# Kernel optimization log

Hardware: AMD Instinct MI355X
Metric: run time of the kernel (lower is better)

The kernel has to match this reference:

```python
import jax, jax.numpy as jnp
import numpy as np

N_NODES = 100000
N_EDGES = 1600000
F_IN, F_HID, F_OUT = 256, 128, 32


def setup_inputs() -> dict:
    key = jax.random.key(0)
    k1, k2, k3, k4 = jax.random.split(key, 4)
    x = jax.random.normal(k1, (N_NODES, F_IN), dtype=jnp.float32)
    edge_index = jax.random.randint(k2, (2, N_EDGES), 0, N_NODES, dtype=jnp.int64)
    W1 = jax.random.normal(k3, (F_IN, F_HID), dtype=jnp.float32) * (1.0 / np.sqrt(F_IN))
    b1 = jnp.zeros((F_HID,), dtype=jnp.float32)
    W2 = jax.random.normal(k4, (F_HID, F_OUT), dtype=jnp.float32) * (1.0 / np.sqrt(F_HID))
    b2 = jnp.zeros((F_OUT,), dtype=jnp.float32)
    return {"x": x, "edge_index": edge_index, "W1": W1, "b1": b1, "W2": W2, "b2": b2}


def _gcn_norm(edge_index, num_nodes):
    # Add self-loops, then symmetric normalization deg^-1/2[src] * deg^-1/2[dst].
    loops = jnp.arange(num_nodes, dtype=edge_index.dtype)
    src = jnp.concatenate([edge_index[0], loops])
    dst = jnp.concatenate([edge_index[1], loops])
    deg = jax.ops.segment_sum(jnp.ones_like(dst, dtype=jnp.float32), dst,
                              num_segments=num_nodes)
    dinv = jnp.where(deg > 0, jax.lax.rsqrt(deg), 0.0)
    norm = dinv[src] * dinv[dst]  # [E + N]
    return src, dst, norm


def _gcn_conv(h, src, dst, norm, num_nodes):
    # h already linearly transformed. Gather sources, scale, scatter-add to dst.
    msgs = h[src] * norm[:, None]
    return jax.ops.segment_sum(msgs, dst, num_segments=num_nodes)


def reference(x, edge_index, W1, b1, W2, b2):
    n = x.shape[0]
    src, dst, norm = _gcn_norm(edge_index, n)
    # Layer 1: linear -> normalized scatter-add -> bias -> relu
    h = _gcn_conv(x @ W1, src, dst, norm, n) + b1
    h = jax.nn.relu(h)
    # F.dropout with training=False (eval mode) is identity.
    # Layer 2
    out = _gcn_conv(h @ W2, src, dst, norm, n) + b2
    return jax.nn.log_softmax(out, axis=1)
```

## Files before the change

kernel.cpp:

```cpp
#include <hip/hip_runtime.h>

#define N_NODES 100000
#define N_EDGES 1600000
#define F_IN 256
#define F_HID 128
#define F_OUT 32
#define NBUCK 391
#define BIN_BLOCKS 512
#define EDGES_PER_BIN 3125
#define G1_BLOCKS 1563

typedef unsigned short ushort_t;
typedef unsigned int uint_t;

using short8  = __attribute__((ext_vector_type(8))) short;
using floatx4 = __attribute__((ext_vector_type(4))) float;

__device__ __forceinline__ ushort_t f2bf(float f) {
    uint_t u = __float_as_uint(f);
    u += 0x7fff + ((u >> 16) & 1);
    return (ushort_t)(u >> 16);
}
__device__ __forceinline__ float bf_lo(uint_t u) { return __uint_as_float(u << 16); }
__device__ __forceinline__ float bf_hi(uint_t u) { return __uint_as_float(u & 0xffff0000u); }
__device__ __forceinline__ uint_t bfpack_trunc(float a, float b) {
    return __builtin_amdgcn_perm(__float_as_uint(b), __float_as_uint(a), 0x07060302u);
}

__global__ __launch_bounds__(256) void histwt_kernel(const int* __restrict__ ei,
                                                     int* __restrict__ bucket_cnt,
                                                     const float* __restrict__ W1,
                                                     const float* __restrict__ W2,
                                                     ushort_t* __restrict__ W1T,
                                                     ushort_t* __restrict__ W2T) {
    __shared__ int h[NBUCK];
    if (blockIdx.x < BIN_BLOCKS) {
        for (int i = threadIdx.x; i < NBUCK; i += 256) h[i] = 0;
        __syncthreads();
        int gid = blockIdx.x * 256 + threadIdx.x;
        for (int e = gid; e < N_EDGES; e += BIN_BLOCKS * 256)
            atomicAdd(&h[ei[N_EDGES + e] >> 8], 1);
        __syncthreads();
        for (int i = threadIdx.x; i < NBUCK; i += 256) {
            int c = h[i];
            if (c) atomicAdd(&bucket_cnt[i], c);
        }
    } else {
        int t = (blockIdx.x - BIN_BLOCKS) * 256 + threadIdx.x;
#pragma unroll
        for (int j = 0; j < 4; j++) {
            int e = j * 8192 + t;
            int n = e >> 8, k = e & 255;
            W1T[e] = f2bf(W1[k * F_HID + n]);
        }
        if (t < 4096) {
            int n = t >> 7, k = t & 127;
            W2T[t] = f2bf(W2[k * F_OUT + n]);
        }
    }
}

__global__ __launch_bounds__(512) void scan_kernel(const int* __restrict__ bucket_cnt,
                                                   int* __restrict__ bucket_base,
                                                   int* __restrict__ bucket_cursor,
                                                   int* __restrict__ offs) {
    __shared__ int s[512];
    int t = threadIdx.x;
    int own = (t < NBUCK) ? bucket_cnt[t] : 0;
    s[t] = own;
    __syncthreads();
    for (int off = 1; off < 512; off <<= 1) {
        int v = (t >= off) ? s[t - off] : 0;
        __syncthreads();
        s[t] += v;
        __syncthreads();
    }
    if (t < NBUCK) {
        int ex = s[t] - own;
        bucket_base[t] = ex;
        bucket_cursor[t] = ex;
    }
    if (t == 0) {
        bucket_base[NBUCK] = N_EDGES;
        offs[N_NODES] = N_EDGES;
    }
}

__global__ __launch_bounds__(256) void bin_gemm1_kernel(const int* __restrict__ ei,
                                                        int* __restrict__ bucket_cursor,
                                                        int2* __restrict__ binned,
                                                        const float* __restrict__ x,
                                                        const ushort_t* __restrict__ W1T,
                                                        ushort_t* __restrict__ h0a,
                                                        ushort_t* __restrict__ h0b) {
    __shared__ __align__(16) char smem[(size_t)F_HID * 136 * 2];
    const int tid = threadIdx.x;
    if (blockIdx.x < BIN_BLOCKS) {
        int* h    = (int*)smem;
        int* base = ((int*)smem) + NBUCK;
        const int beg = blockIdx.x * EDGES_PER_BIN;
        const int end = beg + EDGES_PER_BIN;
        for (int i = tid; i < NBUCK; i += 256) h[i] = 0;
        __syncthreads();
        for (int e = beg + tid; e < end; e += 256) atomicAdd(&h[ei[N_EDGES + e] >> 8], 1);
        __syncthreads();
        for (int i = tid; i < NBUCK; i += 256) {
            int c = h[i];
            base[i] = c ? atomicAdd(&bucket_cursor[i], c) : 0;
            h[i] = 0;
        }
        __syncthreads();
        for (int e = beg + tid; e < end; e += 256) {
            int s = ei[e], d = ei[N_EDGES + e];
            int bk = d >> 8;
            int p = base[bk] + atomicAdd(&h[bk], 1);
            binned[p] = make_int2(s, d);
        }
    } else {
        ushort_t (*Bst)[136] = (ushort_t(*)[136])smem;
        const int rbase = (blockIdx.x - BIN_BLOCKS) * 64;
        const int w = tid >> 6;
        const int lane = tid & 63;
        const int q = lane >> 4;
        const int nloc = lane & 15;

        const int rowA = rbase + w * 16 + nloc;
        const bool okA = rowA < N_NODES;
        const float* ap = x + (size_t)rowA * F_IN + q * 8;

        floatx4 acc[8];
#pragma unroll
        for (int t = 0; t < 8; t++) acc[t] = (floatx4){0.f, 0.f, 0.f, 0.f};

#pragma unroll
        for (int half = 0; half < 2; half++) {
#pragma unroll
            for (int j = 0; j < 8; j++) {
                int f = j * 256 + tid;
                int n = f >> 4, kg = f & 15;
                uint4 v = ((const uint4*)(W1T + n * F_IN + half * 128))[kg];
                *(uint4*)(&Bst[n][kg * 8]) = v;
            }
            __syncthreads();

#pragma unroll
            for (int k0 = 0; k0 < 128; k0 += 32) {
                float4 f0 = make_float4(0.f, 0.f, 0.f, 0.f);
                float4 f1 = make_float4(0.f, 0.f, 0.f, 0.f);
                if (okA) {
                    f0 = *(const float4*)(ap + half * 128 + k0);
                    f1 = *(const float4*)(ap + half * 128 + k0 + 4);
                }
                uint4 au;
                au.x = bfpack_trunc(f0.x, f0.y);
                au.y = bfpack_trunc(f0.z, f0.w);
                au.z = bfpack_trunc(f1.x, f1.y);
                au.w = bfpack_trunc(f1.z, f1.w);
                short8 a = *(short8*)&au;
#pragma unroll
                for (int t = 0; t < 8; t++) {
                    short8 b = *(const short8*)(&Bst[t * 16 + nloc][k0 + q * 8]);
                    acc[t] = __builtin_amdgcn_mfma_f32_16x16x32_bf16(a, b, acc[t], 0, 0, 0);
                }
            }
            __syncthreads();
        }

#pragma unroll
        for (int reg = 0; reg < 4; reg++) {
            int rowD = rbase + w * 16 + q * 4 + reg;
            if (rowD < N_NODES) {
                ushort_t* opA = h0a + (size_t)rowD * 64 + nloc;
                ushort_t* opB = h0b + (size_t)rowD * 64 + nloc;
#pragma unroll
                for (int t = 0; t < 4; t++) opA[t * 16] = f2bf(acc[t][reg]);
#pragma unroll
                for (int t = 4; t < 8; t++) opB[(t - 4) * 16] = f2bf(acc[t][reg]);
            }
        }
    }
}

__global__ __launch_bounds__(256) void build_kernel(const int2* __restrict__ binned,
                                                    const int* __restrict__ bucket_base,
                                                    int* __restrict__ offs,
                                                    int* __restrict__ csr,
                                                    float* __restrict__ dinv,
                                                    int* __restrict__ degarr) {
    __shared__ int h[256];
    __shared__ int sc[256];
    __shared__ int cur[256];
    const int b = blockIdx.x, t = threadIdx.x;
    const int beg = bucket_base[b];
    const int end = bucket_base[b + 1];
    h[t] = 0;
    __syncthreads();
    for (int j = beg + t; j < end; j += 256) {
        int2 p = binned[j];
        atomicAdd(&h[p.y & 255], 1);
    }
    __syncthreads();
    int deg = h[t];
    sc[t] = deg;
    __syncthreads();
    for (int off = 1; off < 256; off <<= 1) {
        int v = (t >= off) ? sc[t - off] : 0;
        __syncthreads();
        sc[t] += v;
        __syncthreads();
    }
    int excl = sc[t] - deg;
    cur[t] = excl;
    int node = b * 256 + t;
    if (node < N_NODES) {
        offs[node] = beg + excl;
        dinv[node] = rsqrtf((float)deg + 1.0f);
        degarr[node] = deg;
    }
    __syncthreads();
    for (int j = beg + t; j < end; j += 256) {
        int2 p = binned[j];
        int pos = atomicAdd(&cur[p.y & 255], 1);
        csr[beg + pos] = p.x;
    }
}

__global__ __launch_bounds__(256) void pack_kernel(int* __restrict__ csr,
                                                   const int* __restrict__ degarr) {
    int i = blockIdx.x * 256 + threadIdx.x;
    if (i >= N_EDGES / 4) return;
    int4 c = ((int4*)csr)[i];
    c.x |= degarr[c.x] << 20;
    c.y |= degarr[c.y] << 20;
    c.z |= degarr[c.z] << 20;
    c.w |= degarr[c.w] << 20;
    ((int4*)csr)[i] = c;
}

__global__ __launch_bounds__(256) void gather64(const ushort_t* __restrict__ h0a,
                                                const ushort_t* __restrict__ h0b,
                                                const int* __restrict__ offs,
                                                const int* __restrict__ csr,
                                                const float* __restrict__ dinv,
                                                ushort_t* __restrict__ aggA,
                                                ushort_t* __restrict__ aggB) {
    const int half = blockIdx.x >= (N_NODES / 8);
    const int nb = blockIdx.x - half * (N_NODES / 8);
    const ushort_t* tab = half ? h0b : h0a;
    ushort_t* outt = half ? aggB : aggA;

    const int node = nb * 8 + (threadIdx.x >> 5);
    const int l = threadIdx.x & 31;
    const int sub = l >> 3;
    const int fl = l & 7;
    const float dn = dinv[node];
    const uint4* rowbase = (const uint4*)tab;

    uint4 sv = rowbase[(size_t)node * 8 + fl];
    float s = (sub == 0) ? dn * dn : 0.f;
    float a[8];
    a[0] = bf_lo(sv.x) * s; a[1] = bf_hi(sv.x) * s;
    a[2] = bf_lo(sv.y) * s; a[3] = bf_hi(sv.y) * s;
    a[4] = bf_lo(sv.z) * s; a[5] = bf_hi(sv.z) * s;
    a[6] = bf_lo(sv.w) * s; a[7] = bf_hi(sv.w) * s;

    const int beg = offs[node], end = offs[node + 1];
    for (int j = beg; j < end; j += 16) {
        uint_t w[4];
        float nn[4];
        uint4 r[4];
#pragma unroll
        for (int k = 0; k < 4; k++) w[k] = ((const uint_t*)csr)[j + 4 * k + sub];
#pragma unroll
        for (int k = 0; k < 4; k++) {
            bool v = (j + 4 * k + sub) < end;
            int src = v ? (int)(w[k] & 0xFFFFFu) : 0;
            nn[k] = v ? rsqrtf((float)(w[k] >> 20) + 1.0f) * dn : 0.f;
            r[k] = rowbase[(size_t)src * 8 + fl];
        }
#pragma unroll
        for (int k = 0; k < 4; k++) {
            float n = nn[k];
            a[0] += bf_lo(r[k].x) * n; a[1] += bf_hi(r[k].x) * n;
            a[2] += bf_lo(r[k].y) * n; a[3] += bf_hi(r[k].y) * n;
            a[4] += bf_lo(r[k].z) * n; a[5] += bf_hi(r[k].z) * n;
            a[6] += bf_lo(r[k].w) * n; a[7] += bf_hi(r[k].w) * n;
        }
    }
#pragma unroll
    for (int i = 0; i < 8; i++) {
        a[i] += __shfl_xor(a[i], 8);
        a[i] += __shfl_xor(a[i], 16);
    }
    if (sub == 0) {
        uint4 p;
        p.x = (uint_t)f2bf(a[0]) | ((uint_t)f2bf(a[1]) << 16);
        p.y = (uint_t)f2bf(a[2]) | ((uint_t)f2bf(a[3]) << 16);
        p.z = (uint_t)f2bf(a[4]) | ((uint_t)f2bf(a[5]) << 16);
        p.w = (uint_t)f2bf(a[6]) | ((uint_t)f2bf(a[7]) << 16);
        ((uint4*)outt)[(size_t)node * 8 + fl] = p;
    }
}

__global__ __launch_bounds__(256) void gemm2_kernel(const ushort_t* __restrict__ aggA,
                                                    const ushort_t* __restrict__ aggB,
                                                    const float* __restrict__ b1,
                                                    const ushort_t* __restrict__ W2T,
                                                    ushort_t* __restrict__ h2bf) {
    __shared__ ushort_t Bs[F_OUT][F_HID + 8];
    __shared__ float b1s[F_HID];
    const int tid = threadIdx.x;
    const int rbase = blockIdx.x * 64;
    const int w = tid >> 6;
    const int lane = tid & 63;
    const int q = lane >> 4;
    const int nloc = lane & 15;

    if (tid < F_HID) b1s[tid] = b1[tid];
#pragma unroll
    for (int jj = 0; jj < 2; jj++) {
        int f = jj * 256 + tid;
        int n = f >> 4, kg = f & 15;
        uint4 v = ((const uint4*)(W2T + n * F_HID))[kg];
        *(uint4*)(&Bs[n][kg * 8]) = v;
    }
    __syncthreads();

    const int rowA = rbase + w * 16 + nloc;
    const bool okA = rowA < N_NODES;

    floatx4 acc[2];
    acc[0] = (floatx4){0.f, 0.f, 0.f, 0.f};
    acc[1] = (floatx4){0.f, 0.f, 0.f, 0.f};

#pragma unroll
    for (int k0 = 0; k0 < F_HID; k0 += 32) {
        int kk = k0 + q * 8;
        const ushort_t* at = (k0 < 64) ? aggA : aggB;
        int kloc = (k0 < 64) ? kk : kk - 64;
        uint4 av = make_uint4(0, 0, 0, 0);
        if (okA) av = *(const uint4*)(at + (size_t)rowA * 64 + kloc);
        float4 bb0 = *(const float4*)(&b1s[kk]);
        float4 bb1 = *(const float4*)(&b1s[kk + 4]);
        uint4 au;
        au.x = bfpack_trunc(fmaxf(bf_lo(av.x) + bb0.x, 0.f), fmaxf(bf_hi(av.x) + bb0.y, 0.f));
        au.y = bfpack_trunc(fmaxf(bf_lo(av.y) + bb0.z, 0.f), fmaxf(bf_hi(av.y) + bb0.w, 0.f));
        au.z = bfpack_trunc(fmaxf(bf_lo(av.z) + bb1.x, 0.f), fmaxf(bf_hi(av.z) + bb1.y, 0.f));
        au.w = bfpack_trunc(fmaxf(bf_lo(av.w) + bb1.z, 0.f), fmaxf(bf_hi(av.w) + bb1.w, 0.f));
        short8 a = *(short8*)&au;
#pragma unroll
        for (int t = 0; t < 2; t++) {
            short8 b = *(const short8*)(&Bs[t * 16 + nloc][kk]);
            acc[t] = __builtin_amdgcn_mfma_f32_16x16x32_bf16(a, b, acc[t], 0, 0, 0);
        }
    }
#pragma unroll
    for (int reg = 0; reg < 4; reg++) {
        int rowD = rbase + w * 16 + q * 4 + reg;
        if (rowD < N_NODES) {
            ushort_t* op = h2bf + (size_t)rowD * F_OUT + nloc;
            op[0]  = f2bf(acc[0][reg]);
            op[16] = f2bf(acc[1][reg]);
        }
    }
}

__global__ __launch_bounds__(256) void gather32_lsm(const ushort_t* __restrict__ h2bf,
                                                    const int* __restrict__ offs,
                                                    const int* __restrict__ csr,
                                                    const float* __restrict__ dinv,
                                                    const float* __restrict__ b2,
                                                    float* __restrict__ out) {
    const int node = blockIdx.x * 8 + (threadIdx.x >> 5);
    const int l = threadIdx.x & 31;
    const int sub = l >> 2;
    const int fl = l & 3;
    const float dn = dinv[node];
    const uint4* rowbase = (const uint4*)h2bf;

    uint4 sv = rowbase[(size_t)node * 4 + fl];
    float s = (sub == 0) ? dn * dn : 0.f;
    float a[8];
    a[0] = bf_lo(sv.x) * s; a[1] = bf_hi(sv.x) * s;
    a[2] = bf_lo(sv.y) * s; a[3] = bf_hi(sv.y) * s;
    a[4] = bf_lo(sv.z) * s; a[5] = bf_hi(sv.z) * s;
    a[6] = bf_lo(sv.w) * s; a[7] = bf_hi(sv.w) * s;

    const int beg = offs[node], end = offs[node + 1];
    for (int j = beg; j < end; j += 16) {
        uint_t w[2];
        float nn[2];
        uint4 r[2];
#pragma unroll
        for (int k = 0; k < 2; k++) w[k] = ((const uint_t*)csr)[j + 8 * k + sub];
#pragma unroll
        for (int k = 0; k < 2; k++) {
            bool v = (j + 8 * k + sub) < end;
            int src = v ? (int)(w[k] & 0xFFFFFu) : 0;
            nn[k] = v ? rsqrtf((float)(w[k] >> 20) + 1.0f) * dn : 0.f;
            r[k] = rowbase[(size_t)src * 4 + fl];
        }
#pragma unroll
        for (int k = 0; k < 2; k++) {
            float n = nn[k];
            a[0] += bf_lo(r[k].x) * n; a[1] += bf_hi(r[k].x) * n;
            a[2] += bf_lo(r[k].y) * n; a[3] += bf_hi(r[k].y) * n;
            a[4] += bf_lo(r[k].z) * n; a[5] += bf_hi(r[k].z) * n;
            a[6] += bf_lo(r[k].w) * n; a[7] += bf_hi(r[k].w) * n;
        }
    }
#pragma unroll
    for (int i = 0; i < 8; i++) {
        a[i] += __shfl_xor(a[i], 4);
        a[i] += __shfl_xor(a[i], 8);
        a[i] += __shfl_xor(a[i], 16);
    }
    float4 bb0 = ((const float4*)b2)[fl * 2];
    float4 bb1 = ((const float4*)b2)[fl * 2 + 1];
    a[0] += bb0.x; a[1] += bb0.y; a[2] += bb0.z; a[3] += bb0.w;
    a[4] += bb1.x; a[5] += bb1.y; a[6] += bb1.z; a[7] += bb1.w;

    float m = a[0];
#pragma unroll
    for (int i = 1; i < 8; i++) m = fmaxf(m, a[i]);
    m = fmaxf(m, __shfl_xor(m, 1));
    m = fmaxf(m, __shfl_xor(m, 2));
    float es = 0.f;
#pragma unroll
    for (int i = 0; i < 8; i++) es += __expf(a[i] - m);
    es += __shfl_xor(es, 1);
    es += __shfl_xor(es, 2);
    float lse = m + __logf(es);

    if (sub == 0) {
        float4 o0 = make_float4(a[0] - lse, a[1] - lse, a[2] - lse, a[3] - lse);
        float4 o1 = make_float4(a[4] - lse, a[5] - lse, a[6] - lse, a[7] - lse);
        float4* op = (float4*)(out + (size_t)node * F_OUT);
        op[fl * 2] = o0;
        op[fl * 2 + 1] = o1;
    }
}

extern "C" void kernel_launch(void* const* d_in, const int* in_sizes, int n_in,
                              void* d_out, int out_size, void* d_ws, size_t ws_size,
                              hipStream_t stream) {
    const float* x  = (const float*)d_in[0];
    const int*   ei = (const int*)d_in[1];
    const float* W1 = (const float*)d_in[2];
    const float* b1 = (const float*)d_in[3];
    const float* W2 = (const float*)d_in[4];
    const float* b2 = (const float*)d_in[5];
    float* out = (float*)d_out;

    float* ws = (float*)d_ws;
    float*    dinv          = ws;
    int*      offs          = (int*)(ws + 100096);
    int*      bucket_cnt    = (int*)(ws + 200224);
    int*      bucket_base   = (int*)(ws + 200736);
    int*      bucket_cursor = (int*)(ws + 201248);
    int*      degarr        = (int*)(ws + 201760);
    int*      csr           = (int*)(ws + 301856);
    ushort_t* W1T           = (ushort_t*)(ws + 1901856);
    ushort_t* W2T           = (ushort_t*)(ws + 1918240);
    ushort_t* h0a           = (ushort_t*)(ws + 1920288);
    ushort_t* h0b           = (ushort_t*)(ws + 5120288);
    ushort_t* aggA          = (ushort_t*)(ws + 8320288);
    ushort_t* aggB          = (ushort_t*)(ws + 11520288);
    ushort_t* h2bf          = (ushort_t*)(ws + 14720288);
    int2*     binned        = (int2*)aggA;

    hipMemsetAsync(bucket_cnt, 0, 512 * sizeof(int), stream);
    histwt_kernel<<<BIN_BLOCKS + 32, 256, 0, stream>>>(ei, bucket_cnt, W1, W2, W1T, W2T);
    scan_kernel<<<1, 512, 0, stream>>>(bucket_cnt, bucket_base, bucket_cursor, offs);
    bin_gemm1_kernel<<<BIN_BLOCKS + G1_BLOCKS, 256, 0, stream>>>(ei, bucket_cursor, binned,
                                                                 x, W1T, h0a, h0b);
    build_kernel<<<NBUCK, 256, 0, stream>>>(binned, bucket_base, offs, csr, dinv, degarr);
    pack_kernel<<<(N_EDGES / 4 + 255) / 256, 256, 0, stream>>>(csr, degarr);
    gather64<<<2 * (N_NODES / 8), 256, 0, stream>>>(h0a, h0b, offs, csr, dinv, aggA, aggB);
    gemm2_kernel<<<(N_NODES + 63) / 64, 256, 0, stream>>>(aggA, aggB, b1, W2T, h2bf);
    gather32_lsm<<<N_NODES / 8, 256, 0, stream>>>(h2bf, offs, csr, dinv, b2, out);
}
```

Measured before the change: 334.0 us.

## Build CSR directly via per-node degree atomics and cursor scatter

Replaces the two-level bucket binning (bucket histogram, binned pair buffer, per-bucket build, separate pack pass) with a per-node global degree histogram, a hierarchical scan, and a direct atomic-cursor scatter into the CSR. The degree is packed into each entry during that scatter. This removes the intermediate binned buffer and the build and pack kernels, cutting memory traffic and launches. In exchange it uses many global atomics on random addresses, and CSR order within a node becomes nondeterministic, which can slightly change float summation order.

```diff
diff --git a/kernel.cpp b/kernel.cpp
--- a/kernel.cpp
+++ b/kernel.cpp
@@ -6,8 +6,7 @@
 #define F_HID 128
 #define F_OUT 32
 #define NBUCK 391
-#define BIN_BLOCKS 512
-#define EDGES_PER_BIN 3125
+#define FILL_BLOCKS 512
 #define G1_BLOCKS 1563
 
 typedef unsigned short ushort_t;
@@ -28,25 +27,17 @@
 }
 
 __global__ __launch_bounds__(256) void histwt_kernel(const int* __restrict__ ei,
-                                                     int* __restrict__ bucket_cnt,
+                                                     int* __restrict__ deg,
                                                      const float* __restrict__ W1,
                                                      const float* __restrict__ W2,
                                                      ushort_t* __restrict__ W1T,
                                                      ushort_t* __restrict__ W2T) {
-    __shared__ int h[NBUCK];
-    if (blockIdx.x < BIN_BLOCKS) {
-        for (int i = threadIdx.x; i < NBUCK; i += 256) h[i] = 0;
-        __syncthreads();
+    if (blockIdx.x < FILL_BLOCKS) {
         int gid = blockIdx.x * 256 + threadIdx.x;
-        for (int e = gid; e < N_EDGES; e += BIN_BLOCKS * 256)
-            atomicAdd(&h[ei[N_EDGES + e] >> 8], 1);
-        __syncthreads();
-        for (int i = threadIdx.x; i < NBUCK; i += 256) {
-            int c = h[i];
-            if (c) atomicAdd(&bucket_cnt[i], c);
-        }
+        for (int e = gid; e < N_EDGES; e += FILL_BLOCKS * 256)
+            atomicAdd(&deg[ei[N_EDGES + e]], 1);
     } else {
-        int t = (blockIdx.x - BIN_BLOCKS) * 256 + threadIdx.x;
+        int t = (blockIdx.x - FILL_BLOCKS) * 256 + threadIdx.x;
 #pragma unroll
         for (int j = 0; j < 4; j++) {
             int e = j * 8192 + t;
@@ -60,9 +51,21 @@
     }
 }
 
+__global__ __launch_bounds__(256) void sum_kernel(const int* __restrict__ deg,
+                                                  int* __restrict__ bucket_cnt) {
+    __shared__ int red[4];
+    const int t = threadIdx.x;
+    int node = blockIdx.x * 256 + t;
+    int v = (node < N_NODES) ? deg[node] : 0;
+#pragma unroll
+    for (int off = 32; off; off >>= 1) v += __shfl_down(v, off);
+    if ((t & 63) == 0) red[t >> 6] = v;
+    __syncthreads();
+    if (t == 0) bucket_cnt[blockIdx.x] = red[0] + red[1] + red[2] + red[3];
+}
+
 __global__ __launch_bounds__(512) void scan_kernel(const int* __restrict__ bucket_cnt,
                                                    int* __restrict__ bucket_base,
-                                                   int* __restrict__ bucket_cursor,
                                                    int* __restrict__ offs) {
     __shared__ int s[512];
     int t = threadIdx.x;
@@ -75,50 +78,55 @@
         s[t] += v;
         __syncthreads();
     }
-    if (t < NBUCK) {
-        int ex = s[t] - own;
-        bucket_base[t] = ex;
-        bucket_cursor[t] = ex;
-    }
-    if (t == 0) {
-        bucket_base[NBUCK] = N_EDGES;
-        offs[N_NODES] = N_EDGES;
-    }
-}
-
-__global__ __launch_bounds__(256) void bin_gemm1_kernel(const int* __restrict__ ei,
-                                                        int* __restrict__ bucket_cursor,
-                                                        int2* __restrict__ binned,
-                                                        const float* __restrict__ x,
-                                                        const ushort_t* __restrict__ W1T,
-                                                        ushort_t* __restrict__ h0a,
-                                                        ushort_t* __restrict__ h0b) {
-    __shared__ __align__(16) char smem[(size_t)F_HID * 136 * 2];
+    if (t < NBUCK) bucket_base[t] = s[t] - own;
+    if (t == 0) offs[N_NODES] = N_EDGES;
+}
+
+__global__ __launch_bounds__(256) void build2_kernel(const int* __restrict__ deg,
+                                                     const int* __restrict__ bucket_base,
+                                                     int* __restrict__ offs,
+                                                     int* __restrict__ cursor,
+                                                     float* __restrict__ dinv) {
+    __shared__ int sc[256];
+    const int b = blockIdx.x, t = threadIdx.x;
+    int node = b * 256 + t;
+    int d = (node < N_NODES) ? deg[node] : 0;
+    sc[t] = d;
+    __syncthreads();
+    for (int off = 1; off < 256; off <<= 1) {
+        int v = (t >= off) ? sc[t - off] : 0;
+        __syncthreads();
+        sc[t] += v;
+        __syncthreads();
+    }
+    int excl = sc[t] - d;
+    if (node < N_NODES) {
+        int o = bucket_base[b] + excl;
+        offs[node] = o;
+        cursor[node] = o;
+        dinv[node] = rsqrtf((float)d + 1.0f);
+    }
+}
+
+__global__ __launch_bounds__(256) void fill_gemm1_kernel(const int* __restrict__ ei,
+                                                         const int* __restrict__ deg,
+                                                         int* __restrict__ cursor,
+                                                         int* __restrict__ csr,
+                                                         const float* __restrict__ x,
+                                                         const ushort_t* __restrict__ W1T,
+                                                         ushort_t* __restrict__ h0a,
+                                                         ushort_t* __restrict__ h0b) {
+    __shared__ __align__(16) ushort_t Bst[F_HID][136];
     const int tid = threadIdx.x;
-    if (blockIdx.x < BIN_BLOCKS) {
-        int* h    = (int*)smem;
-        int* base = ((int*)smem) + NBUCK;
-        const int beg = blockIdx.x * EDGES_PER_BIN;
-        const int end = beg + EDGES_PER_BIN;
-        for (int i = tid; i < NBUCK; i += 256) h[i] = 0;
-        __syncthreads();
-        for (int e = beg + tid; e < end; e += 256) atomicAdd(&h[ei[N_EDGES + e] >> 8], 1);
-        __syncthreads();
-        for (int i = tid; i < NBUCK; i += 256) {
-            int c = h[i];
-            base[i] = c ? atomicAdd(&bucket_cursor[i], c) : 0;
-            h[i] = 0;
-        }
-        __syncthreads();
-        for (int e = beg + tid; e < end; e += 256) {
+    if (blockIdx.x < FILL_BLOCKS) {
+        int gid = blockIdx.x * 256 + tid;
+        for (int e = gid; e < N_EDGES; e += FILL_BLOCKS * 256) {
             int s = ei[e], d = ei[N_EDGES + e];
-            int bk = d >> 8;
-            int p = base[bk] + atomicAdd(&h[bk], 1);
-            binned[p] = make_int2(s, d);
+            int pos = atomicAdd(&cursor[d], 1);
+            csr[pos] = s | (deg[s] << 20);
         }
     } else {
-        ushort_t (*Bst)[136] = (ushort_t(*)[136])smem;
-        const int rbase = (blockIdx.x - BIN_BLOCKS) * 64;
+        const int rbase = (blockIdx.x - FILL_BLOCKS) * 64;
         const int w = tid >> 6;
         const int lane = tid & 63;
         const int q = lane >> 4;
@@ -179,62 +187,6 @@
             }
         }
     }
-}
-
-__global__ __launch_bounds__(256) void build_kernel(const int2* __restrict__ binned,
-                                                    const int* __restrict__ bucket_base,
-                                                    int* __restrict__ offs,
-                                                    int* __restrict__ csr,
-                                                    float* __restrict__ dinv,
-                                                    int* __restrict__ degarr) {
-    __shared__ int h[256];
-    __shared__ int sc[256];
-    __shared__ int cur[256];
-    const int b = blockIdx.x, t = threadIdx.x;
-    const int beg = bucket_base[b];
-    const int end = bucket_base[b + 1];
-    h[t] = 0;
-    __syncthreads();
-    for (int j = beg + t; j < end; j += 256) {
-        int2 p = binned[j];
-        atomicAdd(&h[p.y & 255], 1);
-    }
-    __syncthreads();
-    int deg = h[t];
-    sc[t] = deg;
-    __syncthreads();
-    for (int off = 1; off < 256; off <<= 1) {
-        int v = (t >= off) ? sc[t - off] : 0;
-        __syncthreads();
-        sc[t] += v;
-        __syncthreads();
-    }
-    int excl = sc[t] - deg;
-    cur[t] = excl;
-    int node = b * 256 + t;
-    if (node < N_NODES) {
-        offs[node] = beg + excl;
-        dinv[node] = rsqrtf((float)deg + 1.0f);
-        degarr[node] = deg;
-    }
-    __syncthreads();
-    for (int j = beg + t; j < end; j += 256) {
-        int2 p = binned[j];
-        int pos = atomicAdd(&cur[p.y & 255], 1);
-        csr[beg + pos] = p.x;
-    }
-}
-
-__global__ __launch_bounds__(256) void pack_kernel(int* __restrict__ csr,
-                                                   const int* __restrict__ degarr) {
-    int i = blockIdx.x * 256 + threadIdx.x;
-    if (i >= N_EDGES / 4) return;
-    int4 c = ((int4*)csr)[i];
-    c.x |= degarr[c.x] << 20;
-    c.y |= degarr[c.y] << 20;
-    c.z |= degarr[c.z] << 20;
-    c.w |= degarr[c.w] << 20;
-    ((int4*)csr)[i] = c;
 }
 
 __global__ __launch_bounds__(256) void gather64(const ushort_t* __restrict__ h0a,
@@ -453,29 +405,28 @@
     float* out = (float*)d_out;
 
     float* ws = (float*)d_ws;
-    float*    dinv          = ws;
-    int*      offs          = (int*)(ws + 100096);
-    int*      bucket_cnt    = (int*)(ws + 200224);
-    int*      bucket_base   = (int*)(ws + 200736);
-    int*      bucket_cursor = (int*)(ws + 201248);
-    int*      degarr        = (int*)(ws + 201760);
-    int*      csr           = (int*)(ws + 301856);
-    ushort_t* W1T           = (ushort_t*)(ws + 1901856);
-    ushort_t* W2T           = (ushort_t*)(ws + 1918240);
-    ushort_t* h0a           = (ushort_t*)(ws + 1920288);
-    ushort_t* h0b           = (ushort_t*)(ws + 5120288);
-    ushort_t* aggA          = (ushort_t*)(ws + 8320288);
-    ushort_t* aggB          = (ushort_t*)(ws + 11520288);
-    ushort_t* h2bf          = (ushort_t*)(ws + 14720288);
-    int2*     binned        = (int2*)aggA;
-
-    hipMemsetAsync(bucket_cnt, 0, 512 * sizeof(int), stream);
-    histwt_kernel<<<BIN_BLOCKS + 32, 256, 0, stream>>>(ei, bucket_cnt, W1, W2, W1T, W2T);
-    scan_kernel<<<1, 512, 0, stream>>>(bucket_cnt, bucket_base, bucket_cursor, offs);
-    bin_gemm1_kernel<<<BIN_BLOCKS + G1_BLOCKS, 256, 0, stream>>>(ei, bucket_cursor, binned,
-                                                                 x, W1T, h0a, h0b);
-    build_kernel<<<NBUCK, 256, 0, stream>>>(binned, bucket_base, offs, csr, dinv, degarr);
-    pack_kernel<<<(N_EDGES / 4 + 255) / 256, 256, 0, stream>>>(csr, degarr);
+    float*    dinv        = ws;
+    int*      offs        = (int*)(ws + 100096);
+    int*      degarr      = (int*)(ws + 200224);
+    int*      bucket_cnt  = (int*)(ws + 300320);
+    int*      bucket_base = (int*)(ws + 300832);
+    int*      cursor      = (int*)(ws + 301344);
+    int*      csr         = (int*)(ws + 401440);
+    ushort_t* W1T         = (ushort_t*)(ws + 2001440);
+    ushort_t* W2T         = (ushort_t*)(ws + 2017824);
+    ushort_t* h0a         = (ushort_t*)(ws + 2019872);
+    ushort_t* h0b         = (ushort_t*)(ws + 5219872);
+    ushort_t* aggA        = (ushort_t*)(ws + 8419872);
+    ushort_t* aggB        = (ushort_t*)(ws + 11619872);
+    ushort_t* h2bf        = (ushort_t*)(ws + 14819872);
+
+    hipMemsetAsync(degarr, 0, (100096 + 512) * sizeof(int), stream);
+    histwt_kernel<<<FILL_BLOCKS + 32, 256, 0, stream>>>(ei, degarr, W1, W2, W1T, W2T);
+    sum_kernel<<<NBUCK, 256, 0, stream>>>(degarr, bucket_cnt);
+    scan_kernel<<<1, 512, 0, stream>>>(bucket_cnt, bucket_base, offs);
+    build2_kernel<<<NBUCK, 256, 0, stream>>>(degarr, bucket_base, offs, cursor, dinv);
+    fill_gemm1_kernel<<<FILL_BLOCKS + G1_BLOCKS, 256, 0, stream>>>(ei, degarr, cursor, csr,
+                                                                   x, W1T, h0a, h0b);
     gather64<<<2 * (N_NODES / 8), 256, 0, stream>>>(h0a, h0b, offs, csr, dinv, aggA, aggB);
     gemm2_kernel<<<(N_NODES + 63) / 64, 256, 0, stream>>>(aggA, aggB, b1, W2T, h2bf);
     gather32_lsm<<<N_NODES / 8, 256, 0, stream>>>(h2bf, offs, csr, dinv, b2, out);
```

Result: slower. 403.2 us (+20.7%).
